# Optimization experiments

Hardware: AMD Instinct MI355X
Metric: run time of the kernel (lower is better)

Reference implementation:

```python
import jax, jax.numpy as jnp
import numpy as np

DIM = 192; EXP = 2; QKB = 4
INNER = EXP * DIM          # 384
NH = INNER // QKB          # 96 heads
DH = QKB                   # 4 dims per head
Hs, Ws = 24, 24; S = Hs * Ws; B = 1; K = 3
EPS = 1e-6


def setup_inputs() -> dict:
    key = jax.random.key(0)
    ks = jax.random.split(key, 16)
    sm_up = (2.0 / (5.0 * DIM)) ** 0.5
    sm_dn = (2.0 / (5.0 * INNER)) ** 0.5
    def n(k, shape, s):
        return jax.random.normal(k, shape, jnp.float32) * s
    return {
        "x": jax.random.normal(ks[0], (B, S, DIM), jnp.float32),
        "d": jax.random.normal(ks[1], (B, S, DIM), jnp.float32),
        "ln_w": jnp.ones((DIM,), jnp.float32),
        "ln_b": jnp.zeros((DIM,), jnp.float32),
        "up_w": n(ks[2], (2 * INNER, DIM), sm_up),
        "up_b": jnp.zeros((2 * INNER,), jnp.float32),
        "dup_w": n(ks[3], (INNER, DIM), sm_up),
        "dup_b": jnp.zeros((INNER,), jnp.float32),
        "q_w": n(ks[4], (NH, DH, DH), sm_up), "q_b": jnp.zeros((INNER,), jnp.float32),
        "k_w": n(ks[5], (NH, DH, DH), sm_up), "k_b": jnp.zeros((INNER,), jnp.float32),
        "v_w": n(ks[6], (NH, DH, DH), sm_up), "v_b": jnp.zeros((INNER,), jnp.float32),
        "conv_w": n(ks[7], (INNER, K, K), 0.1), "conv_b": jnp.zeros((INNER,), jnp.float32),
        "ig_w": n(ks[8], (NH, 3 * INNER), 0.01),
        "ig_b": jax.random.normal(ks[9], (NH,), jnp.float32) * 0.1 - 3.0,
        "fg_w": jnp.zeros((NH, 3 * INNER), jnp.float32),
        "fg_b": jnp.linspace(3.0, 6.0, NH, dtype=jnp.float32),
        "onorm_w": jnp.ones((INNER,), jnp.float32),
        "skip": jnp.ones((INNER,), jnp.float32),
        "down_w": n(ks[10], (DIM, INNER), sm_dn),
        "down_b": jnp.zeros((DIM,), jnp.float32),
    }


def _headwise(x, w, b):
    # LinearHeadwiseExpand: block-diagonal linear, per-head DHxDH matrix
    Bx, Sx, _ = x.shape
    y = jnp.einsum('bsni,noi->bsno', x.reshape(Bx, Sx, NH, DH), w)
    return y.reshape(Bx, Sx, INNER) + b


def _mlstm(q, k, v, ig, fg, onorm_w):
    # parallel_stabilized_simple: q,k,v [B,NH,S,DH]; ig,fg [B,NH,S]
    Sq = q.shape[2]
    log_f = jax.nn.log_sigmoid(fg)                    # [B,NH,S]
    lfc = jnp.cumsum(log_f, axis=-1)                  # cumulative log forget
    logfm = lfc[..., :, None] - lfc[..., None, :]     # [B,NH,S,S]
    mask = jnp.tril(jnp.ones((Sq, Sq), dtype=bool))
    logD = jnp.where(mask, logfm + ig[..., None, :], -jnp.inf)
    maxD = jnp.max(logD, axis=-1, keepdims=True)      # [B,NH,S,1] stabilizer
    Dm = jnp.exp(logD - maxD)
    C = jnp.einsum('bnsd,bntd->bnst', q, k / (DH ** 0.5)) * Dm
    norm = jnp.maximum(jnp.abs(C.sum(-1, keepdims=True)), jnp.exp(-maxD))
    h = jnp.einsum('bnst,bntd->bnsd', C / (norm + EPS), v)
    # MultiHeadLayerNorm (group norm over DH per head, weight only)
    mu = h.mean(-1, keepdims=True)
    var = h.var(-1, keepdims=True)
    return (h - mu) / jnp.sqrt(var + 1e-5) * onorm_w.reshape(NH, DH)[None, :, None, :]


def _forward(x, d, ln_w, ln_b, up_w, up_b, dup_w, dup_b, q_w, q_b, k_w, k_b,
             v_w, v_b, conv_w, conv_b, ig_w, ig_b, fg_w, fg_b, onorm_w, skip,
             down_w, down_b):
    Bx, Sx, _ = x.shape
    # pre-norm LayerNorm
    mu = x.mean(-1, keepdims=True)
    var = x.var(-1, keepdims=True)
    xn = (x - mu) / jnp.sqrt(var + 1e-5) * ln_w + ln_b
    x_inner = xn @ up_w.T + up_b                      # [B,S,2*INNER]
    x_mlstm, z = jnp.split(x_inner, 2, axis=-1)
    d_mlstm = d @ dup_w.T + dup_b                     # dead code in original forward
    # depthwise 3x3 conv over the HxW token grid (SequenceConv2d, groups=INNER)
    kern = jnp.transpose(conv_w, (1, 2, 0))[:, :, None, :]   # HWIO
    xc = jax.lax.conv_general_dilated(
        x_mlstm.reshape(Bx, Hs, Ws, INNER), kern, (1, 1), 'SAME',
        dimension_numbers=('NHWC', 'HWIO', 'NHWC'),
        feature_group_count=INNER) + conv_b
    xa = jax.nn.silu(xc.reshape(Bx, Sx, INNER))
    q = _headwise(xa, q_w, q_b)
    k = _headwise(xa, k_w, k_b)
    v = _headwise(x_mlstm, v_w, v_b)
    gin = jnp.concatenate([q, k, v], axis=-1)         # [B,S,3*INNER]
    ig = (gin @ ig_w.T + ig_b).transpose(0, 2, 1)     # [B,NH,S]
    fg = (gin @ fg_w.T + fg_b).transpose(0, 2, 1)
    to_h = lambda t: t.reshape(Bx, Sx, NH, DH).transpose(0, 2, 1, 3)
    h = _mlstm(to_h(q), to_h(k), to_h(v), ig, fg, onorm_w)   # [B,NH,S,DH]
    h = h.transpose(0, 2, 1, 3).reshape(Bx, Sx, INNER)
    h = (h + skip * xa) * jax.nn.silu(z)
    return h @ down_w.T + down_b


def reference(x, d, ln_w, ln_b, up_w, up_b, dup_w, dup_b, q_w, q_b, k_w, k_b,
              v_w, v_b, conv_w, conv_b, ig_w, ig_b, fg_w, fg_b, onorm_w, skip,
              down_w, down_b):
    return _forward(x, d, ln_w, ln_b, up_w, up_b, dup_w, dup_b, q_w, q_b,
                    k_w, k_b, v_w, v_b, conv_w, conv_b, ig_w, ig_b, fg_w,
                    fg_b, onorm_w, skip, down_w, down_b)
```

## Files before the change

### kernel.cpp

```cpp
#include <hip/hip_runtime.h>
#include <math.h>

#define SEQ 576
#define DIM 192
#define INNER 384
#define NHEAD 96
#define HS 24
#define WSZ 24
#define GKS 4

__global__ __launch_bounds__(256) void k_up(const float* __restrict__ x,
    const float* __restrict__ lnw, const float* __restrict__ lnb,
    const float* __restrict__ w, const float* __restrict__ b,
    float* __restrict__ out) {
  int m0 = blockIdx.x * 64, n0 = blockIdx.y * 32;
  __shared__ float As[DIM * 64];
  __shared__ float Bs[DIM * 32];
  __shared__ float mu[64], inv[64], ps[192];
  int t = threadIdx.x;
  for (int idx = t; idx < 64 * 48; idx += 256) {
    int r = idx / 48, k4 = idx % 48;
    float4 v = *(const float4*)&x[(m0 + r) * DIM + 4 * k4];
    int rw = r ^ (4 * (k4 & 15));
    As[(4 * k4 + 0) * 64 + rw] = v.x;
    As[(4 * k4 + 1) * 64 + rw] = v.y;
    As[(4 * k4 + 2) * 64 + rw] = v.z;
    As[(4 * k4 + 3) * 64 + rw] = v.w;
  }
  for (int idx = t; idx < 32 * 48; idx += 256) {
    int r = idx / 48, k4 = idx % 48;
    float4 v = *(const float4*)&w[(n0 + r) * DIM + 4 * k4];
    int rw = r ^ (4 * (k4 & 7));
    Bs[(4 * k4 + 0) * 32 + rw] = v.x;
    Bs[(4 * k4 + 1) * 32 + rw] = v.y;
    Bs[(4 * k4 + 2) * 32 + rw] = v.z;
    Bs[(4 * k4 + 3) * 32 + rw] = v.w;
  }
  __syncthreads();
  if (t < 192) {
    int r = t % 64, ph = t / 64;
    float s_ = 0.f;
    #pragma unroll 8
    for (int k = ph * 64; k < ph * 64 + 64; ++k)
      s_ += As[k * 64 + (r ^ (4 * ((k >> 2) & 15)))];
    ps[t] = s_;
  }
  __syncthreads();
  if (t < 64) mu[t] = (ps[t] + ps[64 + t] + ps[128 + t]) * (1.0f / DIM);
  __syncthreads();
  if (t < 192) {
    int r = t % 64, ph = t / 64;
    float m_ = mu[r], s_ = 0.f;
    #pragma unroll 8
    for (int k = ph * 64; k < ph * 64 + 64; ++k) {
      float d = As[k * 64 + (r ^ (4 * ((k >> 2) & 15)))] - m_;
      s_ += d * d;
    }
    ps[t] = s_;
  }
  __syncthreads();
  if (t < 64) inv[t] = rsqrtf((ps[t] + ps[64 + t] + ps[128 + t]) * (1.0f / DIM) + 1e-5f);
  __syncthreads();
  for (int idx = t; idx < 64 * DIM; idx += 256) {
    int k = idx >> 6, r0 = idx & 63;
    int m = r0 ^ (4 * ((k >> 2) & 15));
    As[idx] = (As[idx] - mu[m]) * inv[m] * lnw[k] + lnb[k];
  }
  __syncthreads();
  int gm = t >> 4, gn = t & 15;
  float acc[4][2];
  #pragma unroll
  for (int i = 0; i < 4; ++i)
    #pragma unroll
    for (int j = 0; j < 2; ++j) acc[i][j] = b[n0 + 2 * gn + j];
  #pragma unroll 4
  for (int kk = 0; kk < DIM; ++kk) {
    int mk = (kk >> 2) & 15, nk = 4 * ((kk >> 2) & 7);
    float4 a = *(const float4*)&As[kk * 64 + 4 * (gm ^ mk)];
    float2 bv = *(const float2*)&Bs[kk * 32 + ((2 * gn) ^ nk)];
    acc[0][0] += a.x * bv.x; acc[0][1] += a.x * bv.y;
    acc[1][0] += a.y * bv.x; acc[1][1] += a.y * bv.y;
    acc[2][0] += a.z * bv.x; acc[2][1] += a.z * bv.y;
    acc[3][0] += a.w * bv.x; acc[3][1] += a.w * bv.y;
  }
  #pragma unroll
  for (int i = 0; i < 4; ++i)
    *(float2*)&out[(m0 + 4 * gm + i) * (2 * INNER) + n0 + 2 * gn] =
        make_float2(acc[i][0], acc[i][1]);
}

__global__ __launch_bounds__(384) void k_cqkv(const float* __restrict__ xin,
    const float* __restrict__ cw, const float* __restrict__ cb,
    const float* __restrict__ igw, const float* __restrict__ fgw,
    const float* __restrict__ qw, const float* __restrict__ kw,
    const float* __restrict__ vw,
    float* __restrict__ xa, float* __restrict__ xaT,
    float* __restrict__ xmT, float* __restrict__ weff) {
  int s = blockIdx.x, t = threadIdx.x;
  int h = s / WSZ, wc = s % WSZ;
  float acc = cb[t];
  #pragma unroll
  for (int kh = 0; kh < 3; ++kh) {
    int hh = h + kh - 1;
    if (hh < 0 || hh >= HS) continue;
    #pragma unroll
    for (int kw2 = 0; kw2 < 3; ++kw2) {
      int ww = wc + kw2 - 1;
      if (ww < 0 || ww >= WSZ) continue;
      acc += xin[(hh * WSZ + ww) * (2 * INNER) + t] * cw[t * 9 + kh * 3 + kw2];
    }
  }
  float sil = acc / (1.0f + __expf(-acc));
  xa[s * INNER + t] = sil;
  xaT[t * SEQ + s] = sil;
  xmT[t * SEQ + s] = xin[s * (2 * INNER) + t];
  if (s < 192) {
    const float* wg = (s < NHEAD) ? (igw + s * 1152) : (fgw + (s - NHEAD) * 1152);
    for (int cp = t; cp < 768; cp += 384) {
      float wv = 0.f;
      if (cp < 384) {
        int n = cp >> 2, j = cp & 3;
        #pragma unroll
        for (int o = 0; o < 4; ++o)
          wv += wg[4 * n + o] * qw[n * 16 + o * 4 + j]
              + wg[384 + 4 * n + o] * kw[n * 16 + o * 4 + j];
      } else {
        int c2 = cp - 384;
        int n = c2 >> 2, j = c2 & 3;
        #pragma unroll
        for (int o = 0; o < 4; ++o)
          wv += wg[768 + 4 * n + o] * vw[n * 16 + o * 4 + j];
      }
      weff[s * 768 + cp] = wv;
    }
  }
}

#define GBK 192
__global__ __launch_bounds__(256) void k_gates(const float* __restrict__ gT,
    const float* __restrict__ weff,
    float* __restrict__ pig, float* __restrict__ pfg) {
  int m0 = blockIdx.x * 32, s0 = blockIdx.y * 64, ksl = blockIdx.z;
  int k0 = ksl * GBK;
  const float* wb = weff + m0 * 768;
  __shared__ float Ws[GBK * 32];
  __shared__ float Gs[GBK * 64];
  int t = threadIdx.x;
  for (int idx = t; idx < 32 * 48; idx += 256) {
    int r = idx / 48, k4 = idx % 48;
    float4 v = *(const float4*)&wb[r * 768 + k0 + 4 * k4];
    int rw = r ^ (4 * (k4 & 7));
    Ws[(4 * k4 + 0) * 32 + rw] = v.x;
    Ws[(4 * k4 + 1) * 32 + rw] = v.y;
    Ws[(4 * k4 + 2) * 32 + rw] = v.z;
    Ws[(4 * k4 + 3) * 32 + rw] = v.w;
  }
  for (int idx = t; idx < GBK * 16; idx += 256) {
    int kk = idx / 16, s4 = idx % 16;
    *(float4*)&Gs[kk * 64 + 4 * s4] =
        *(const float4*)&gT[(k0 + kk) * SEQ + s0 + 4 * s4];
  }
  __syncthreads();
  int gm = t >> 4, gn = t & 15;
  float acc[2][4] = {{0.f,0.f,0.f,0.f},{0.f,0.f,0.f,0.f}};
  #pragma unroll 4
  for (int kk = 0; kk < GBK; ++kk) {
    int nk = 4 * ((kk >> 2) & 7);
    float2 wv = *(const float2*)&Ws[kk * 32 + ((2 * gm) ^ nk)];
    float4 gv = *(const float4*)&Gs[kk * 64 + 4 * gn];
    acc[0][0] += wv.x * gv.x; acc[0][1] += wv.x * gv.y;
    acc[0][2] += wv.x * gv.z; acc[0][3] += wv.x * gv.w;
    acc[1][0] += wv.y * gv.x; acc[1][1] += wv.y * gv.y;
    acc[1][2] += wv.y * gv.z; acc[1][3] += wv.y * gv.w;
  }
  #pragma unroll
  for (int i = 0; i < 2; ++i) {
    int mm = m0 + 2 * gm + i;
    float* dst = (mm < NHEAD) ? (pig + ksl * NHEAD * SEQ + mm * SEQ)
                              : (pfg + ksl * NHEAD * SEQ + (mm - NHEAD) * SEQ);
    *(float4*)&dst[s0 + 4 * gn] =
        make_float4(acc[i][0], acc[i][1], acc[i][2], acc[i][3]);
  }
}

__global__ __launch_bounds__(576) void k_mlstm(const float* __restrict__ xaT,
    const float* __restrict__ xmT,
    const float* __restrict__ pig, const float* __restrict__ pfg,
    const float* __restrict__ igw, const float* __restrict__ fgw,
    const float* __restrict__ igb, const float* __restrict__ fgb,
    const float* __restrict__ qw, const float* __restrict__ kw,
    const float* __restrict__ vw,
    const float* __restrict__ qb, const float* __restrict__ kb,
    const float* __restrict__ vb,
    const float* __restrict__ onw, float* __restrict__ hout) {
  int n = blockIdx.x, hh = blockIdx.y, t = threadIdx.x;
  int base = 288 * hh;
  int cnt2 = base + 288;
  __shared__ float ksm[SEQ * 4], vsm[SEQ * 4], esm[SEQ];
  __shared__ float qsm[288 * 4];
  __shared__ float lfcs[SEQ], pms[SEQ];
  __shared__ float wsum[16], wmax[16], bdi[16], bdf[16];
  const int H4 = NHEAD * SEQ;
  int lane = t & 63, w = t >> 6;
  {
    float b1 = (t < 384) ? qb[t] : kb[t - 384];
    float b2 = (t < 192) ? kb[192 + t] : vb[t - 192];
    float w1 = igw[n * 1152 + t], w2 = igw[n * 1152 + 576 + t];
    float f1 = fgw[n * 1152 + t], f2 = fgw[n * 1152 + 576 + t];
    float pi = w1 * b1 + w2 * b2;
    float pf = f1 * b1 + f2 * b2;
    #pragma unroll
    for (int o2 = 32; o2 > 0; o2 >>= 1) {
      pi += __shfl_down(pi, o2);
      pf += __shfl_down(pf, o2);
    }
    if (lane == 0) { bdi[w] = pi; bdf[w] = pf; }
  }
  float psi = 0.f, psf = 0.f;
  if (t < cnt2) {
    const float* xan = xaT + 4 * n * SEQ;
    float a0 = xan[t], a1 = xan[SEQ + t], a2 = xan[2 * SEQ + t], a3 = xan[3 * SEQ + t];
    const float* xmn = xmT + 4 * n * SEQ;
    float m0_ = xmn[t], m1_ = xmn[SEQ + t], m2_ = xmn[2 * SEQ + t], m3_ = xmn[3 * SEQ + t];
    #pragma unroll
    for (int o = 0; o < 4; ++o) {
      float kv = kb[4 * n + o] + kw[n * 16 + o * 4 + 0] * a0 + kw[n * 16 + o * 4 + 1] * a1
               + kw[n * 16 + o * 4 + 2] * a2 + kw[n * 16 + o * 4 + 3] * a3;
      ksm[t * 4 + o] = kv * 0.5f;
      vsm[t * 4 + o] = vb[4 * n + o] + vw[n * 16 + o * 4 + 0] * m0_ + vw[n * 16 + o * 4 + 1] * m1_
               + vw[n * 16 + o * 4 + 2] * m2_ + vw[n * 16 + o * 4 + 3] * m3_;
    }
    if (t >= base) {
      int r = t - base;
      #pragma unroll
      for (int o = 0; o < 4; ++o)
        qsm[r * 4 + o] = qb[4 * n + o] + qw[n * 16 + o * 4 + 0] * a0 + qw[n * 16 + o * 4 + 1] * a1
                 + qw[n * 16 + o * 4 + 2] * a2 + qw[n * 16 + o * 4 + 3] * a3;
    }
    int off = n * SEQ + t;
    psi = pig[off] + pig[off + H4] + pig[off + 2 * H4] + pig[off + 3 * H4];
    psf = pfg[off] + pfg[off + H4] + pfg[off + 2 * H4] + pfg[off + 3 * H4];
  }
  __syncthreads();
  float bdI = bdi[0] + bdi[1] + bdi[2] + bdi[3] + bdi[4] + bdi[5] + bdi[6] + bdi[7] + bdi[8];
  float bdF = bdf[0] + bdf[1] + bdf[2] + bdf[3] + bdf[4] + bdf[5] + bdf[6] + bdf[7] + bdf[8];
  float ai = 0.f, lf = 0.f;
  if (t < cnt2) {
    ai = igb[n] + bdI + psi;
    float af = fgb[n] + bdF + psf;
    lf = (af >= 0.f) ? -log1pf(expf(-af)) : (af - log1pf(expf(af)));
  }
  float v = (t < cnt2) ? lf : 0.f;
  #pragma unroll
  for (int o2 = 1; o2 < 64; o2 <<= 1) {
    float u = __shfl_up(v, o2);
    if (lane >= o2) v += u;
  }
  if (lane == 63) wsum[w] = v;
  __syncthreads();
  if (t < 16) {
    float sv = (t < 9) ? wsum[t] : 0.f;
    #pragma unroll
    for (int o2 = 1; o2 < 16; o2 <<= 1) {
      float u = __shfl_up(sv, o2);
      if (t >= o2) sv += u;
    }
    wsum[t] = sv;
  }
  __syncthreads();
  float lfc = v + ((w > 0) ? wsum[w - 1] : 0.f);
  float e = ai - lfc;
  float m = (t < cnt2) ? e : -3.0e38f;
  #pragma unroll
  for (int o2 = 1; o2 < 64; o2 <<= 1) {
    float u = __shfl_up(m, o2);
    if (lane >= o2) m = fmaxf(m, u);
  }
  if (lane == 63) wmax[w] = m;
  __syncthreads();
  if (t < 16) {
    float sv = (t < 9) ? wmax[t] : -3.0e38f;
    #pragma unroll
    for (int o2 = 1; o2 < 16; o2 <<= 1) {
      float u = __shfl_up(sv, o2);
      if (t >= o2) sv = fmaxf(sv, u);
    }
    wmax[t] = sv;
  }
  __syncthreads();
  float pm = (w > 0) ? fmaxf(m, wmax[w - 1]) : m;
  if (t < cnt2) {
    esm[t] = e;
    lfcs[t] = lfc;
    pms[t] = pm;
  }
  __syncthreads();
  int rq = t >> 3, cq = t & 7;
  int s0 = base + 4 * rq;
  int N = s0 + 4;
  float pmv[4], qv[4][4];
  #pragma unroll
  for (int i = 0; i < 4; ++i) {
    pmv[i] = pms[s0 + i];
    *(float4*)&qv[i][0] = *(float4*)&qsm[(4 * rq + i) * 4];
  }
  int ch = (N + 7) >> 3;
  int lo = cq * ch, hi = min(lo + ch, N);
  float cs[4] = {0.f, 0.f, 0.f, 0.f};
  float hv[4][4];
  #pragma unroll
  for (int i = 0; i < 4; ++i)
    #pragma unroll
    for (int j = 0; j < 4; ++j) hv[i][j] = 0.f;
  for (int tt = lo; tt < hi; ++tt) {
    float e3 = esm[tt];
    float4 kv = *(const float4*)&ksm[tt * 4];
    float4 vv = *(const float4*)&vsm[tt * 4];
    #pragma unroll
    for (int i = 0; i < 4; ++i) {
      if (tt <= s0 + i) {
        float d = __expf(e3 - pmv[i]);
        float c = (qv[i][0] * kv.x + qv[i][1] * kv.y +
                   qv[i][2] * kv.z + qv[i][3] * kv.w) * d;
        cs[i] += c;
        hv[i][0] += c * vv.x; hv[i][1] += c * vv.y;
        hv[i][2] += c * vv.z; hv[i][3] += c * vv.w;
      }
    }
  }
  #pragma unroll
  for (int o2 = 4; o2 > 0; o2 >>= 1) {
    #pragma unroll
    for (int i = 0; i < 4; ++i) {
      cs[i] += __shfl_down(cs[i], o2);
      hv[i][0] += __shfl_down(hv[i][0], o2);
      hv[i][1] += __shfl_down(hv[i][1], o2);
      hv[i][2] += __shfl_down(hv[i][2], o2);
      hv[i][3] += __shfl_down(hv[i][3], o2);
    }
  }
  if (cq == 0) {
    #pragma unroll
    for (int i = 0; i < 4; ++i) {
      int s = s0 + i;
      float mxv = lfcs[s] + pmv[i];
      float norm = fmaxf(fabsf(cs[i]), __expf(-mxv)) + 1e-6f;
      float rr = 1.0f / norm;
      float h0 = hv[i][0] * rr, h1 = hv[i][1] * rr;
      float h2 = hv[i][2] * rr, h3 = hv[i][3] * rr;
      float mu = (h0 + h1 + h2 + h3) * 0.25f;
      float d0 = h0 - mu, d1 = h1 - mu, d2 = h2 - mu, d3 = h3 - mu;
      float var = (d0 * d0 + d1 * d1 + d2 * d2 + d3 * d3) * 0.25f;
      float inv = rsqrtf(var + 1e-5f);
      *(float4*)&hout[s * INNER + n * 4] = make_float4(
          d0 * inv * onw[n * 4 + 0], d1 * inv * onw[n * 4 + 1],
          d2 * inv * onw[n * 4 + 2], d3 * inv * onw[n * 4 + 3]);
    }
  }
}

#define KPA 388
__global__ __launch_bounds__(128) void k_down(const float* __restrict__ hmat,
    const float* __restrict__ xa, const float* __restrict__ xin,
    const float* __restrict__ skip, const float* __restrict__ dw,
    const float* __restrict__ db, float* __restrict__ out) {
  int m0 = blockIdx.x * 16, n0 = blockIdx.y * 32;
  __shared__ float As[16 * KPA];
  __shared__ float Bs[INNER * 32];
  int t = threadIdx.x;
  for (int idx = t; idx < 16 * 96; idx += 128) {
    int r = idx / 96, k4 = idx % 96;
    int s = m0 + r;
    float4 zv = *(const float4*)&xin[s * (2 * INNER) + INNER + 4 * k4];
    float4 hm = *(const float4*)&hmat[s * INNER + 4 * k4];
    float4 xv = *(const float4*)&xa[s * INNER + 4 * k4];
    float4 sk = *(const float4*)&skip[4 * k4];
    float z, sil;
    float4 o;
    z = zv.x; sil = z / (1.0f + __expf(-z)); o.x = (hm.x + sk.x * xv.x) * sil;
    z = zv.y; sil = z / (1.0f + __expf(-z)); o.y = (hm.y + sk.y * xv.y) * sil;
    z = zv.z; sil = z / (1.0f + __expf(-z)); o.z = (hm.z + sk.z * xv.z) * sil;
    z = zv.w; sil = z / (1.0f + __expf(-z)); o.w = (hm.w + sk.w * xv.w) * sil;
    *(float4*)&As[r * KPA + 4 * k4] = o;
  }
  for (int idx = t; idx < 32 * 96; idx += 128) {
    int r = idx / 96, k4 = idx % 96;
    float4 v = *(const float4*)&dw[(n0 + r) * INNER + 4 * k4];
    int rw = r ^ (4 * (k4 & 7));
    Bs[(4 * k4 + 0) * 32 + rw] = v.x;
    Bs[(4 * k4 + 1) * 32 + rw] = v.y;
    Bs[(4 * k4 + 2) * 32 + rw] = v.z;
    Bs[(4 * k4 + 3) * 32 + rw] = v.w;
  }
  __syncthreads();
  int gm = t >> 4, gn = t & 15;
  float acc[2][2];
  #pragma unroll
  for (int i = 0; i < 2; ++i)
    #pragma unroll
    for (int j = 0; j < 2; ++j) acc[i][j] = db[n0 + 2 * gn + j];
  #pragma unroll 4
  for (int kk = 0; kk < INNER; ++kk) {
    int nk = 4 * ((kk >> 2) & 7);
    float a0 = As[(2 * gm) * KPA + kk];
    float a1 = As[(2 * gm + 1) * KPA + kk];
    float2 bv = *(const float2*)&Bs[kk * 32 + ((2 * gn) ^ nk)];
    acc[0][0] += a0 * bv.x; acc[0][1] += a0 * bv.y;
    acc[1][0] += a1 * bv.x; acc[1][1] += a1 * bv.y;
  }
  #pragma unroll
  for (int i = 0; i < 2; ++i)
    *(float2*)&out[(m0 + 2 * gm + i) * DIM + n0 + 2 * gn] =
        make_float2(acc[i][0], acc[i][1]);
}

extern "C" void kernel_launch(void* const* d_in, const int* in_sizes, int n_in,
                              void* d_out, int out_size, void* d_ws, size_t ws_size,
                              hipStream_t stream) {
  const float* x      = (const float*)d_in[0];
  const float* ln_w   = (const float*)d_in[2];
  const float* ln_b   = (const float*)d_in[3];
  const float* up_w   = (const float*)d_in[4];
  const float* up_b   = (const float*)d_in[5];
  const float* q_w    = (const float*)d_in[8];
  const float* q_b    = (const float*)d_in[9];
  const float* k_w    = (const float*)d_in[10];
  const float* k_b    = (const float*)d_in[11];
  const float* v_w    = (const float*)d_in[12];
  const float* v_b    = (const float*)d_in[13];
  const float* conv_w = (const float*)d_in[14];
  const float* conv_b = (const float*)d_in[15];
  const float* ig_w   = (const float*)d_in[16];
  const float* ig_b   = (const float*)d_in[17];
  const float* fg_w   = (const float*)d_in[18];
  const float* fg_b   = (const float*)d_in[19];
  const float* onorm_w= (const float*)d_in[20];
  const float* skip   = (const float*)d_in[21];
  const float* down_w = (const float*)d_in[22];
  const float* down_b = (const float*)d_in[23];
  float* out = (float*)d_out;

  float* ws     = (float*)d_ws;
  float* xinner = ws;
  float* xa     = xinner + SEQ * 2 * INNER;
  float* xaT    = xa + SEQ * INNER;
  float* xmT    = xaT + INNER * SEQ;
  float* weff   = xmT + INNER * SEQ;
  float* pig    = weff + 192 * 768;
  float* pfg    = pig + GKS * NHEAD * SEQ;
  float* hbuf   = pfg + GKS * NHEAD * SEQ;

  k_up   <<<dim3(9, 24), 256, 0, stream>>>(x, ln_w, ln_b, up_w, up_b, xinner);
  k_cqkv <<<SEQ, 384, 0, stream>>>(xinner, conv_w, conv_b, ig_w, fg_w,
                                   q_w, k_w, v_w, xa, xaT, xmT, weff);
  k_gates<<<dim3(6, 9, GKS), 256, 0, stream>>>(xaT, weff, pig, pfg);
  k_mlstm<<<dim3(NHEAD, 2), 576, 0, stream>>>(xaT, xmT, pig, pfg, ig_w, fg_w,
                                              ig_b, fg_b, q_w, k_w, v_w,
                                              q_b, k_b, v_b, onorm_w, hbuf);
  k_down <<<dim3(36, 6), 128, 0, stream>>>(hbuf, xa, xinner, skip, down_w, down_b, out);
}
```

Baseline: 92.60 us.

## Fuse conv+SiLU and transposes into gates GEMM, fold weff into up kernel

Removes the separate k_cqkv launch. The effective gate-weight precompute moves into an extra column of blocks in k_up. The depthwise conv plus SiLU is now computed directly into shared memory inside k_gates, with block column 0 also writing the xa, xaT and xmT buffers. Shared memory gets a padded stride of 68 to reduce bank conflicts. This saves one kernel launch and a global round trip, but each of the 6 gate row-blocks recomputes the conv redundantly.

```diff
diff --git a/kernel.cpp b/kernel.cpp
--- a/kernel.cpp
+++ b/kernel.cpp
@@ -12,111 +12,16 @@
 __global__ __launch_bounds__(256) void k_up(const float* __restrict__ x,
     const float* __restrict__ lnw, const float* __restrict__ lnb,
     const float* __restrict__ w, const float* __restrict__ b,
-    float* __restrict__ out) {
-  int m0 = blockIdx.x * 64, n0 = blockIdx.y * 32;
-  __shared__ float As[DIM * 64];
-  __shared__ float Bs[DIM * 32];
-  __shared__ float mu[64], inv[64], ps[192];
-  int t = threadIdx.x;
-  for (int idx = t; idx < 64 * 48; idx += 256) {
-    int r = idx / 48, k4 = idx % 48;
-    float4 v = *(const float4*)&x[(m0 + r) * DIM + 4 * k4];
-    int rw = r ^ (4 * (k4 & 15));
-    As[(4 * k4 + 0) * 64 + rw] = v.x;
-    As[(4 * k4 + 1) * 64 + rw] = v.y;
-    As[(4 * k4 + 2) * 64 + rw] = v.z;
-    As[(4 * k4 + 3) * 64 + rw] = v.w;
-  }
-  for (int idx = t; idx < 32 * 48; idx += 256) {
-    int r = idx / 48, k4 = idx % 48;
-    float4 v = *(const float4*)&w[(n0 + r) * DIM + 4 * k4];
-    int rw = r ^ (4 * (k4 & 7));
-    Bs[(4 * k4 + 0) * 32 + rw] = v.x;
-    Bs[(4 * k4 + 1) * 32 + rw] = v.y;
-    Bs[(4 * k4 + 2) * 32 + rw] = v.z;
-    Bs[(4 * k4 + 3) * 32 + rw] = v.w;
-  }
-  __syncthreads();
-  if (t < 192) {
-    int r = t % 64, ph = t / 64;
-    float s_ = 0.f;
-    #pragma unroll 8
-    for (int k = ph * 64; k < ph * 64 + 64; ++k)
-      s_ += As[k * 64 + (r ^ (4 * ((k >> 2) & 15)))];
-    ps[t] = s_;
-  }
-  __syncthreads();
-  if (t < 64) mu[t] = (ps[t] + ps[64 + t] + ps[128 + t]) * (1.0f / DIM);
-  __syncthreads();
-  if (t < 192) {
-    int r = t % 64, ph = t / 64;
-    float m_ = mu[r], s_ = 0.f;
-    #pragma unroll 8
-    for (int k = ph * 64; k < ph * 64 + 64; ++k) {
-      float d = As[k * 64 + (r ^ (4 * ((k >> 2) & 15)))] - m_;
-      s_ += d * d;
-    }
-    ps[t] = s_;
-  }
-  __syncthreads();
-  if (t < 64) inv[t] = rsqrtf((ps[t] + ps[64 + t] + ps[128 + t]) * (1.0f / DIM) + 1e-5f);
-  __syncthreads();
-  for (int idx = t; idx < 64 * DIM; idx += 256) {
-    int k = idx >> 6, r0 = idx & 63;
-    int m = r0 ^ (4 * ((k >> 2) & 15));
-    As[idx] = (As[idx] - mu[m]) * inv[m] * lnw[k] + lnb[k];
-  }
-  __syncthreads();
-  int gm = t >> 4, gn = t & 15;
-  float acc[4][2];
-  #pragma unroll
-  for (int i = 0; i < 4; ++i)
-    #pragma unroll
-    for (int j = 0; j < 2; ++j) acc[i][j] = b[n0 + 2 * gn + j];
-  #pragma unroll 4
-  for (int kk = 0; kk < DIM; ++kk) {
-    int mk = (kk >> 2) & 15, nk = 4 * ((kk >> 2) & 7);
-    float4 a = *(const float4*)&As[kk * 64 + 4 * (gm ^ mk)];
-    float2 bv = *(const float2*)&Bs[kk * 32 + ((2 * gn) ^ nk)];
-    acc[0][0] += a.x * bv.x; acc[0][1] += a.x * bv.y;
-    acc[1][0] += a.y * bv.x; acc[1][1] += a.y * bv.y;
-    acc[2][0] += a.z * bv.x; acc[2][1] += a.z * bv.y;
-    acc[3][0] += a.w * bv.x; acc[3][1] += a.w * bv.y;
-  }
-  #pragma unroll
-  for (int i = 0; i < 4; ++i)
-    *(float2*)&out[(m0 + 4 * gm + i) * (2 * INNER) + n0 + 2 * gn] =
-        make_float2(acc[i][0], acc[i][1]);
-}
-
-__global__ __launch_bounds__(384) void k_cqkv(const float* __restrict__ xin,
-    const float* __restrict__ cw, const float* __restrict__ cb,
     const float* __restrict__ igw, const float* __restrict__ fgw,
     const float* __restrict__ qw, const float* __restrict__ kw,
     const float* __restrict__ vw,
-    float* __restrict__ xa, float* __restrict__ xaT,
-    float* __restrict__ xmT, float* __restrict__ weff) {
-  int s = blockIdx.x, t = threadIdx.x;
-  int h = s / WSZ, wc = s % WSZ;
-  float acc = cb[t];
-  #pragma unroll
-  for (int kh = 0; kh < 3; ++kh) {
-    int hh = h + kh - 1;
-    if (hh < 0 || hh >= HS) continue;
-    #pragma unroll
-    for (int kw2 = 0; kw2 < 3; ++kw2) {
-      int ww = wc + kw2 - 1;
-      if (ww < 0 || ww >= WSZ) continue;
-      acc += xin[(hh * WSZ + ww) * (2 * INNER) + t] * cw[t * 9 + kh * 3 + kw2];
-    }
-  }
-  float sil = acc / (1.0f + __expf(-acc));
-  xa[s * INNER + t] = sil;
-  xaT[t * SEQ + s] = sil;
-  xmT[t * SEQ + s] = xin[s * (2 * INNER) + t];
-  if (s < 192) {
-    const float* wg = (s < NHEAD) ? (igw + s * 1152) : (fgw + (s - NHEAD) * 1152);
-    for (int cp = t; cp < 768; cp += 384) {
+    float* __restrict__ out, float* __restrict__ weff) {
+  int t = threadIdx.x;
+  if (blockIdx.x == 9) {
+    int r0 = blockIdx.y * 8;
+    for (int idx = t; idx < 8 * 768; idx += 256) {
+      int r = r0 + idx / 768, cp = idx % 768;
+      const float* wg = (r < NHEAD) ? (igw + r * 1152) : (fgw + (r - NHEAD) * 1152);
       float wv = 0.f;
       if (cp < 384) {
         int n = cp >> 2, j = cp & 3;
@@ -131,43 +36,149 @@
         for (int o = 0; o < 4; ++o)
           wv += wg[768 + 4 * n + o] * vw[n * 16 + o * 4 + j];
       }
-      weff[s * 768 + cp] = wv;
-    }
-  }
+      weff[r * 768 + cp] = wv;
+    }
+    return;
+  }
+  int m0 = blockIdx.x * 64, n0 = blockIdx.y * 32;
+  __shared__ float As[DIM * 64];
+  __shared__ float Bs[DIM * 32];
+  __shared__ float mu[64], inv[64], ps[192];
+  for (int idx = t; idx < 64 * 48; idx += 256) {
+    int r = idx / 48, k4 = idx % 48;
+    float4 v = *(const float4*)&x[(m0 + r) * DIM + 4 * k4];
+    int rw = r ^ (4 * (k4 & 15));
+    As[(4 * k4 + 0) * 64 + rw] = v.x;
+    As[(4 * k4 + 1) * 64 + rw] = v.y;
+    As[(4 * k4 + 2) * 64 + rw] = v.z;
+    As[(4 * k4 + 3) * 64 + rw] = v.w;
+  }
+  for (int idx = t; idx < 32 * 48; idx += 256) {
+    int r = idx / 48, k4 = idx % 48;
+    float4 v = *(const float4*)&w[(n0 + r) * DIM + 4 * k4];
+    int rw = r ^ (4 * (k4 & 7));
+    Bs[(4 * k4 + 0) * 32 + rw] = v.x;
+    Bs[(4 * k4 + 1) * 32 + rw] = v.y;
+    Bs[(4 * k4 + 2) * 32 + rw] = v.z;
+    Bs[(4 * k4 + 3) * 32 + rw] = v.w;
+  }
+  __syncthreads();
+  if (t < 192) {
+    int r = t % 64, ph = t / 64;
+    float s_ = 0.f;
+    #pragma unroll 8
+    for (int k = ph * 64; k < ph * 64 + 64; ++k)
+      s_ += As[k * 64 + (r ^ (4 * ((k >> 2) & 15)))];
+    ps[t] = s_;
+  }
+  __syncthreads();
+  if (t < 64) mu[t] = (ps[t] + ps[64 + t] + ps[128 + t]) * (1.0f / DIM);
+  __syncthreads();
+  if (t < 192) {
+    int r = t % 64, ph = t / 64;
+    float m_ = mu[r], s_ = 0.f;
+    #pragma unroll 8
+    for (int k = ph * 64; k < ph * 64 + 64; ++k) {
+      float d = As[k * 64 + (r ^ (4 * ((k >> 2) & 15)))] - m_;
+      s_ += d * d;
+    }
+    ps[t] = s_;
+  }
+  __syncthreads();
+  if (t < 64) inv[t] = rsqrtf((ps[t] + ps[64 + t] + ps[128 + t]) * (1.0f / DIM) + 1e-5f);
+  __syncthreads();
+  for (int idx = t; idx < 64 * DIM; idx += 256) {
+    int k = idx >> 6, r0 = idx & 63;
+    int m = r0 ^ (4 * ((k >> 2) & 15));
+    As[idx] = (As[idx] - mu[m]) * inv[m] * lnw[k] + lnb[k];
+  }
+  __syncthreads();
+  int gm = t >> 4, gn = t & 15;
+  float acc[4][2];
+  #pragma unroll
+  for (int i = 0; i < 4; ++i)
+    #pragma unroll
+    for (int j = 0; j < 2; ++j) acc[i][j] = b[n0 + 2 * gn + j];
+  #pragma unroll 4
+  for (int kk = 0; kk < DIM; ++kk) {
+    int mk = (kk >> 2) & 15, nk = 4 * ((kk >> 2) & 7);
+    float4 a = *(const float4*)&As[kk * 64 + 4 * (gm ^ mk)];
+    float2 bv = *(const float2*)&Bs[kk * 32 + ((2 * gn) ^ nk)];
+    acc[0][0] += a.x * bv.x; acc[0][1] += a.x * bv.y;
+    acc[1][0] += a.y * bv.x; acc[1][1] += a.y * bv.y;
+    acc[2][0] += a.z * bv.x; acc[2][1] += a.z * bv.y;
+    acc[3][0] += a.w * bv.x; acc[3][1] += a.w * bv.y;
+  }
+  #pragma unroll
+  for (int i = 0; i < 4; ++i)
+    *(float2*)&out[(m0 + 4 * gm + i) * (2 * INNER) + n0 + 2 * gn] =
+        make_float2(acc[i][0], acc[i][1]);
 }
 
 #define GBK 192
-__global__ __launch_bounds__(256) void k_gates(const float* __restrict__ gT,
+#define GP 68
+__global__ __launch_bounds__(256) void k_gates(const float* __restrict__ xinner,
+    const float* __restrict__ cw, const float* __restrict__ cb,
     const float* __restrict__ weff,
+    float* __restrict__ xa, float* __restrict__ xaT, float* __restrict__ xmT,
     float* __restrict__ pig, float* __restrict__ pfg) {
-  int m0 = blockIdx.x * 32, s0 = blockIdx.y * 64, ksl = blockIdx.z;
-  int k0 = ksl * GBK;
-  const float* wb = weff + m0 * 768;
+  int bx = blockIdx.x, s0 = blockIdx.y * 64, bz = blockIdx.z;
+  int m0 = bx * 32, k0 = bz * GBK;
   __shared__ float Ws[GBK * 32];
-  __shared__ float Gs[GBK * 64];
+  __shared__ float Gs[GBK * GP];
   int t = threadIdx.x;
   for (int idx = t; idx < 32 * 48; idx += 256) {
     int r = idx / 48, k4 = idx % 48;
-    float4 v = *(const float4*)&wb[r * 768 + k0 + 4 * k4];
+    float4 v = *(const float4*)&weff[(m0 + r) * 768 + k0 + 4 * k4];
     int rw = r ^ (4 * (k4 & 7));
     Ws[(4 * k4 + 0) * 32 + rw] = v.x;
     Ws[(4 * k4 + 1) * 32 + rw] = v.y;
     Ws[(4 * k4 + 2) * 32 + rw] = v.z;
     Ws[(4 * k4 + 3) * 32 + rw] = v.w;
   }
-  for (int idx = t; idx < GBK * 16; idx += 256) {
-    int kk = idx / 16, s4 = idx % 16;
-    *(float4*)&Gs[kk * 64 + 4 * s4] =
-        *(const float4*)&gT[(k0 + kk) * SEQ + s0 + 4 * s4];
-  }
-  __syncthreads();
+  if (bz < 2) {
+    for (int idx = t; idx < 64 * GBK; idx += 256) {
+      int ss = idx / GBK, cl = idx % GBK;
+      int s = s0 + ss, h = s / WSZ, wc = s % WSZ;
+      int C = k0 + cl;
+      float acc = cb[C];
+      #pragma unroll
+      for (int kh = 0; kh < 3; ++kh) {
+        int hh = h + kh - 1;
+        if (hh < 0 || hh >= HS) continue;
+        #pragma unroll
+        for (int kw2 = 0; kw2 < 3; ++kw2) {
+          int ww = wc + kw2 - 1;
+          if (ww < 0 || ww >= WSZ) continue;
+          acc += xinner[(hh * WSZ + ww) * (2 * INNER) + C] * cw[C * 9 + kh * 3 + kw2];
+        }
+      }
+      float sil = acc / (1.0f + __expf(-acc));
+      Gs[cl * GP + ss] = sil;
+      if (bx == 0) xa[s * INNER + C] = sil;
+    }
+  } else {
+    int cbase = (bz - 2) * GBK;
+    for (int idx = t; idx < 64 * GBK; idx += 256) {
+      int ss = idx / GBK, cl = idx % GBK;
+      Gs[cl * GP + ss] = xinner[(s0 + ss) * (2 * INNER) + cbase + cl];
+    }
+  }
+  __syncthreads();
+  if (bx == 0) {
+    float* dstT = (bz < 2) ? (xaT + k0 * SEQ) : (xmT + (bz - 2) * GBK * SEQ);
+    for (int idx = t; idx < GBK * 64; idx += 256) {
+      int cl = idx >> 6, ss = idx & 63;
+      dstT[cl * SEQ + s0 + ss] = Gs[cl * GP + ss];
+    }
+  }
   int gm = t >> 4, gn = t & 15;
   float acc[2][4] = {{0.f,0.f,0.f,0.f},{0.f,0.f,0.f,0.f}};
   #pragma unroll 4
   for (int kk = 0; kk < GBK; ++kk) {
     int nk = 4 * ((kk >> 2) & 7);
     float2 wv = *(const float2*)&Ws[kk * 32 + ((2 * gm) ^ nk)];
-    float4 gv = *(const float4*)&Gs[kk * 64 + 4 * gn];
+    float4 gv = *(const float4*)&Gs[kk * GP + 4 * gn];
     acc[0][0] += wv.x * gv.x; acc[0][1] += wv.x * gv.y;
     acc[0][2] += wv.x * gv.z; acc[0][3] += wv.x * gv.w;
     acc[1][0] += wv.y * gv.x; acc[1][1] += wv.y * gv.y;
@@ -176,8 +187,8 @@
   #pragma unroll
   for (int i = 0; i < 2; ++i) {
     int mm = m0 + 2 * gm + i;
-    float* dst = (mm < NHEAD) ? (pig + ksl * NHEAD * SEQ + mm * SEQ)
-                              : (pfg + ksl * NHEAD * SEQ + (mm - NHEAD) * SEQ);
+    float* dst = (mm < NHEAD) ? (pig + bz * NHEAD * SEQ + mm * SEQ)
+                              : (pfg + bz * NHEAD * SEQ + (mm - NHEAD) * SEQ);
     *(float4*)&dst[s0 + 4 * gn] =
         make_float4(acc[i][0], acc[i][1], acc[i][2], acc[i][3]);
   }
@@ -450,10 +461,11 @@
   float* pfg    = pig + GKS * NHEAD * SEQ;
   float* hbuf   = pfg + GKS * NHEAD * SEQ;
 
-  k_up   <<<dim3(9, 24), 256, 0, stream>>>(x, ln_w, ln_b, up_w, up_b, xinner);
-  k_cqkv <<<SEQ, 384, 0, stream>>>(xinner, conv_w, conv_b, ig_w, fg_w,
-                                   q_w, k_w, v_w, xa, xaT, xmT, weff);
-  k_gates<<<dim3(6, 9, GKS), 256, 0, stream>>>(xaT, weff, pig, pfg);
+  k_up   <<<dim3(10, 24), 256, 0, stream>>>(x, ln_w, ln_b, up_w, up_b,
+                                            ig_w, fg_w, q_w, k_w, v_w,
+                                            xinner, weff);
+  k_gates<<<dim3(6, 9, GKS), 256, 0, stream>>>(xinner, conv_w, conv_b, weff,
+                                               xa, xaT, xmT, pig, pfg);
   k_mlstm<<<dim3(NHEAD, 2), 576, 0, stream>>>(xaT, xmT, pig, pfg, ig_w, fg_w,
                                               ig_b, fg_b, q_w, k_w, v_w,
                                               q_b, k_b, v_b, onorm_w, hbuf);
```

Measured after the change: 150.9 us. +63.0%, slower.
